# Kernel tuning notes

Measured on AMD Instinct MI355X. Metric: run time of the kernel, lower is better.

The kernel has to match this reference:

```python
import jax, jax.numpy as jnp
import numpy as np

N, E, D, L = 100000, 1600000, 128, 4
NEG_SLOPE = 0.2
LOGSTD_MAX = 10.0


def setup_inputs() -> dict:
    key = jax.random.key(0)
    ks = jax.random.split(key, 20)
    s = 1.0 / np.sqrt(D)
    inp = {
        "x": jax.random.normal(ks[0], (N, D), jnp.float32),
        "edge_index": jax.random.randint(ks[1], (2, E), 0, N, dtype=jnp.int32),
        "eps": jax.random.normal(ks[2], (N, D), jnp.float32),
        # encoder GATv2 stack (4 layers, all inc=D)
        "enc_Wl": jax.random.normal(ks[3], (L, D, D), jnp.float32) * s,
        "enc_Wr": jax.random.normal(ks[4], (L, D, D), jnp.float32) * s,
        "enc_att": jax.random.normal(ks[5], (L, D), jnp.float32) * s,
        "enc_b": jnp.zeros((L, D), jnp.float32),
        # decoder GATv2 stack
        "dec_Wl": jax.random.normal(ks[6], (L, D, D), jnp.float32) * s,
        "dec_Wr": jax.random.normal(ks[7], (L, D, D), jnp.float32) * s,
        "dec_att": jax.random.normal(ks[8], (L, D), jnp.float32) * s,
        "dec_b": jnp.zeros((L, D), jnp.float32),
        # VAE heads
        "W_mu": jax.random.normal(ks[9], (D, D), jnp.float32) * s,
        "b_mu": jnp.zeros((D,), jnp.float32),
        "W_ls": jax.random.normal(ks[10], (D, D), jnp.float32) * s,
        "b_ls": jnp.zeros((D,), jnp.float32),
        # attribute reconstruction head and degree predictor
        "W_out": jax.random.normal(ks[11], (D, D), jnp.float32) * s,
        "b_out": jnp.zeros((D,), jnp.float32),
        "W_deg": jax.random.normal(ks[12], (D, 1), jnp.float32) * s,
        "b_deg": jnp.zeros((1,), jnp.float32),
    }
    return inp


def _gatv2_stack(h, src, dst, Wl, Wr, att, b):
    """Stack of GATv2Conv (heads=1) + gelu, PyG semantics (softmax over incoming edges of dst)."""
    for l in range(Wl.shape[0]):
        xl = h @ Wl[l]  # [N, D] source-side transform
        xr = h @ Wr[l]  # [N, D] target-side transform
        # per-edge GATv2 score: a^T LeakyReLU(xl_j + xr_i)
        e = jax.nn.leaky_relu(xl[src] + xr[dst], NEG_SLOPE) @ att[l]  # [E+N]
        m = jax.ops.segment_max(e, dst, num_segments=N)
        w = jnp.exp(e - m[dst])
        denom = jax.ops.segment_sum(w, dst, num_segments=N)
        alpha = w / denom[dst]
        h = jax.ops.segment_sum(alpha[:, None] * xl[src], dst, num_segments=N) + b[l]
        h = jax.nn.gelu(h, approximate=False)  # torch F.gelu default = exact erf
    return h


def reference(x, edge_index, eps, enc_Wl, enc_Wr, enc_att, enc_b,
              dec_Wl, dec_Wr, dec_att, dec_b,
              W_mu, b_mu, W_ls, b_ls, W_out, b_out, W_deg, b_deg):
    loops = jnp.arange(N, dtype=edge_index.dtype)
    src = jnp.concatenate([edge_index[0], loops])  # add self loops (GATv2Conv default)
    dst = jnp.concatenate([edge_index[1], loops])

    h = _gatv2_stack(x, src, dst, enc_Wl, enc_Wr, enc_att, enc_b)
    mu = h @ W_mu + b_mu
    logstd = jnp.minimum(h @ W_ls + b_ls, LOGSTD_MAX)
    z = mu + eps * jnp.exp(logstd)

    h_dec = _gatv2_stack(z, src, dst, dec_Wl, dec_Wr, dec_att, dec_b)
    x_rec = h_dec @ W_out + b_out
    degree_pred = (z @ W_deg + b_deg)[:, 0]
    return x_rec, z, mu, logstd, degree_pred
```

## Files before the change

kernel.cpp:

```cpp
#include <hip/hip_runtime.h>
#include <math.h>

#define NN 100000
#define MPAD 100096
#define DD 128
#define EE 1600000
#define ET (EE + NN)
#define ND (NN * DD)

#define NBKT 782
#define IPB 16384
#define GSC 104
#define BCAP 6144

typedef short bf16x8 __attribute__((ext_vector_type(8)));
typedef float f32x4 __attribute__((ext_vector_type(4)));

static __device__ __forceinline__ unsigned short f2bf(float f) {
  unsigned int u = __float_as_uint(f);
  u += 0x7FFFu + ((u >> 16) & 1u);
  return (unsigned short)(u >> 16);
}
static __device__ __forceinline__ float bf2f(unsigned short h) {
  return __uint_as_float(((unsigned int)h) << 16);
}
static __device__ __forceinline__ float gelu_exact(float v) {
  return 0.5f * v * (1.f + erff(v * 0.7071067811865476f));
}


__global__ void k_zero_int(int* __restrict__ p, int n) {
  int i = blockIdx.x * blockDim.x + threadIdx.x;
  if (i < n) p[i] = 0;
}

__global__ __launch_bounds__(256) void kb_hist(const int* __restrict__ ei,
                                               int* __restrict__ cnt) {
  __shared__ int lc[NBKT];
  int t = threadIdx.x;
  for (int b = t; b < NBKT; b += 256) lc[b] = 0;
  __syncthreads();
  int i0 = blockIdx.x * IPB;
  int i1 = min(i0 + IPB, ET);
  for (int i = i0 + t; i < i1; i += 256) {
    int dst = (i < EE) ? ei[EE + i] : (i - EE);
    atomicAdd(&lc[dst >> 7], 1);
  }
  __syncthreads();
  for (int b = t; b < NBKT; b += 256) {
    int c = lc[b];
    if (c) atomicAdd(&cnt[b], c);
  }
}

__global__ __launch_bounds__(256) void kb_scan(const int* __restrict__ cnt,
                                               int* __restrict__ off,
                                               int* __restrict__ cur) {
  __shared__ int sh[256];
  int t = threadIdx.x;
  int c[4]; int s = 0;
#pragma unroll
  for (int j = 0; j < 4; ++j) {
    int b = t * 4 + j;
    c[j] = s;
    int v = (b < NBKT) ? cnt[b] : 0;
    s += v;
  }
  sh[t] = s; __syncthreads();
  for (int o = 1; o < 256; o <<= 1) {
    int v = (t >= o) ? sh[t - o] : 0;
    __syncthreads();
    sh[t] += v;
    __syncthreads();
  }
  int excl = sh[t] - s;
#pragma unroll
  for (int j = 0; j < 4; ++j) {
    int b = t * 4 + j;
    if (b < NBKT) { off[b] = excl + c[j]; cur[b] = excl + c[j]; }
  }
  if (t == 255) off[NBKT] = excl + s;
}

__global__ __launch_bounds__(256) void kb_scatter(const int* __restrict__ ei,
                                                  int* __restrict__ cur,
                                                  int* __restrict__ buf) {
  __shared__ int lc[NBKT];
  __shared__ int lb[NBKT];
  int t = threadIdx.x;
  for (int b = t; b < NBKT; b += 256) lc[b] = 0;
  __syncthreads();
  int i0 = blockIdx.x * IPB;
  int i1 = min(i0 + IPB, ET);
  for (int i = i0 + t; i < i1; i += 256) {
    int dst = (i < EE) ? ei[EE + i] : (i - EE);
    atomicAdd(&lc[dst >> 7], 1);
  }
  __syncthreads();
  for (int b = t; b < NBKT; b += 256) {
    int c = lc[b];
    lb[b] = c ? atomicAdd(&cur[b], c) : 0;
    lc[b] = 0;
  }
  __syncthreads();
  for (int i = i0 + t; i < i1; i += 256) {
    int src, dst;
    if (i < EE) { src = ei[i]; dst = ei[EE + i]; } else { src = i - EE; dst = src; }
    int b = dst >> 7;
    int l = atomicAdd(&lc[b], 1);
    buf[lb[b] + l] = src | ((dst & 127) << 17);
  }
}

__global__ __launch_bounds__(256) void kb_fin(const int* __restrict__ buf,
                                              const int* __restrict__ off,
                                              int* __restrict__ csr_src,
                                              int* __restrict__ row_ptr) {
  __shared__ int ebuf[BCAP];
  __shared__ int osrc[BCAP];
  __shared__ int cnt[128], scn[128], lcur[128];
  int b = blockIdx.x;
  int base = off[b];
  int count = min(off[b + 1] - base, BCAP);
  int t = threadIdx.x;
  if (t < 128) { cnt[t] = 0; lcur[t] = 0; }
  __syncthreads();
  for (int i = t; i < count; i += 256) {
    int w = buf[base + i];
    ebuf[i] = w;
    atomicAdd(&cnt[(w >> 17) & 127], 1);
  }
  __syncthreads();
  if (t < 128) scn[t] = cnt[t];
  __syncthreads();
  for (int o = 1; o < 128; o <<= 1) {
    int v = 0;
    if (t < 128 && t >= o) v = scn[t - o];
    __syncthreads();
    if (t < 128) scn[t] += v;
    __syncthreads();
  }
  for (int i = t; i < count; i += 256) {
    int w = ebuf[i];
    int d = (w >> 17) & 127;
    int l = atomicAdd(&lcur[d], 1);
    osrc[(scn[d] - cnt[d]) + l] = w & 0x1FFFF;
  }
  __syncthreads();
  for (int i = t; i < count; i += 256) csr_src[base + i] = osrc[i];
  if (t < 128) {
    int gd = b * 128 + t;
    if (gd <= NN) row_ptr[gd] = base + scn[t] - cnt[t];
  }
}


__global__ __launch_bounds__(256) void k_wconv(const float* __restrict__ encWl,
                                               const float* __restrict__ encWr,
                                               const float* __restrict__ decWl,
                                               const float* __restrict__ decWr,
                                               const float* __restrict__ Wmu,
                                               const float* __restrict__ Wls,
                                               const float* __restrict__ Wout,
                                               unsigned short* __restrict__ wfh,
                                               unsigned short* __restrict__ wfl) {
  int wid = (blockIdx.x * 256 + threadIdx.x) >> 6;
  int lane = threadIdx.x & 63;
  if (wid >= 19 * 32) return;
  int mat = wid >> 5;
  int sub = wid & 31;
  const float* W;
  if (mat < 4) W = encWl + (size_t)mat * 16384;
  else if (mat < 8) W = encWr + (size_t)(mat - 4) * 16384;
  else if (mat < 12) W = decWl + (size_t)(mat - 8) * 16384;
  else if (mat < 16) W = decWr + (size_t)(mat - 12) * 16384;
  else if (mat == 16) W = Wmu;
  else if (mat == 17) W = Wls;
  else W = Wout;
  int t = sub >> 3, c = sub & 7;
  int col = c * 16 + (lane & 15);
  int k0 = t * 32 + (lane >> 4) * 8;
  bf16x8 vh, vl;
#pragma unroll
  for (int j = 0; j < 8; ++j) {
    float w = W[(size_t)(k0 + j) * 128 + col];
    unsigned short h = f2bf(w);
    vh[j] = (short)h;
    vl[j] = (short)f2bf(w - bf2f(h));
  }
  size_t base = ((size_t)wid * 64 + lane) * 8;
  *(bf16x8*)(wfh + base) = vh;
  *(bf16x8*)(wfl + base) = vl;
}


__global__ void k_xconv(const float* __restrict__ x, unsigned short* __restrict__ sh) {
  int i = blockIdx.x * blockDim.x + threadIdx.x;
  if (i >= MPAD * 128 / 8) return;
  size_t base = (size_t)i * 8;
  float v[8];
  if (base < (size_t)ND) {
    float4 f0 = *(const float4*)(x + base);
    float4 f1 = *(const float4*)(x + base + 4);
    v[0] = f0.x; v[1] = f0.y; v[2] = f0.z; v[3] = f0.w;
    v[4] = f1.x; v[5] = f1.y; v[6] = f1.z; v[7] = f1.w;
  } else {
#pragma unroll
    for (int j = 0; j < 8; ++j) v[j] = 0.f;
  }
  bf16x8 vh;
#pragma unroll
  for (int j = 0; j < 8; ++j) vh[j] = (short)f2bf(v[j]);
  *(bf16x8*)(sh + base) = vh;
}


__global__ __launch_bounds__(512, 4) void k_mmL(const unsigned short* __restrict__ Ah,
                                                const unsigned short* __restrict__ w1,
                                                const unsigned short* __restrict__ w2,
                                                unsigned short* __restrict__ o1,
                                                unsigned short* __restrict__ o2) {
  __shared__ float lds[128 * 132];
  unsigned short* lw = (unsigned short*)lds;
  int tid = threadIdx.x;
  {
    int4* d = (int4*)lw;
    const int4* s1 = (const int4*)w1;
    const int4* s2 = (const int4*)w2;
#pragma unroll
    for (int i = 0; i < 4; ++i) {
      d[tid + i * 512] = s1[tid + i * 512];
      d[2048 + tid + i * 512] = s2[tid + i * 512];
    }
  }
  int wv = tid >> 6, lane = tid & 63;
  int lrow = lane & 15, lk = lane >> 4;
  int rbase = blockIdx.x * 128 + wv * 16;

  bf16x8 a_h[4];
  const unsigned short* ap = Ah + (size_t)(rbase + lrow) * 128 + lk * 8;
#pragma unroll
  for (int t = 0; t < 4; ++t) a_h[t] = *(const bf16x8*)(ap + t * 32);
  __syncthreads();

  f32x4 acc1[8], acc2[8];
#pragma unroll
  for (int c = 0; c < 8; ++c) {
    acc1[c] = (f32x4){0.f, 0.f, 0.f, 0.f};
    acc2[c] = (f32x4){0.f, 0.f, 0.f, 0.f};
  }
#pragma unroll
  for (int t = 0; t < 4; ++t) {
#pragma unroll
    for (int c = 0; c < 8; ++c) {
      int fo = ((t * 8 + c) * 64 + lane) * 8;
      bf16x8 wf1 = *(const bf16x8*)(lw + fo);
      bf16x8 wf2 = *(const bf16x8*)(lw + 16384 + fo);
      acc1[c] = __builtin_amdgcn_mfma_f32_16x16x32_bf16(a_h[t], wf1, acc1[c], 0, 0, 0);
      acc2[c] = __builtin_amdgcn_mfma_f32_16x16x32_bf16(a_h[t], wf2, acc2[c], 0, 0, 0);
    }
  }
  __syncthreads();

  int lr = tid >> 2, cb = (tid & 3) << 5;
  size_t o = ((size_t)blockIdx.x * 128 + lr) * 128 + cb;

#pragma unroll
  for (int out = 0; out < 2; ++out) {
#pragma unroll
    for (int c = 0; c < 8; ++c)
#pragma unroll
      for (int r = 0; r < 4; ++r)
        lds[(wv * 16 + lk * 4 + r) * 132 + c * 16 + lrow] = out ? acc2[c][r] : acc1[c][r];
    __syncthreads();
    {
      unsigned short* dst = out ? o2 : o1;
      const float* sp = &lds[lr * 132 + cb];
#pragma unroll
      for (int i = 0; i < 4; ++i) {
        union { unsigned short u[8]; int4 v; } pk;
#pragma unroll
        for (int j = 0; j < 8; ++j) pk.u[j] = f2bf(sp[i * 8 + j]);
        *(int4*)&dst[o + i * 8] = pk.v;
      }
    }
    __syncthreads();
  }
}


__global__ __launch_bounds__(512, 3) void k_mmH(const unsigned short* Ah,
                                                const unsigned short* Al,
                                                const unsigned short* __restrict__ w1h,
                                                const unsigned short* __restrict__ w1l,
                                                const unsigned short* __restrict__ w2h,
                                                const unsigned short* __restrict__ w2l,
                                                const float* __restrict__ b1,
                                                const float* __restrict__ b2,
                                                const float* __restrict__ eps,
                                                const float* __restrict__ Wd,
                                                const float* __restrict__ bd,
                                                float* __restrict__ mu,
                                                float* __restrict__ logstd,
                                                float* __restrict__ Z,
                                                unsigned short* Zh,
                                                float* __restrict__ degp) {
  __shared__ float lds[128 * 132];
  unsigned short* lw = (unsigned short*)lds;
  int tid = threadIdx.x;
  int wv = tid >> 6, lane = tid & 63;
  int lrow = lane & 15, lk = lane >> 4;
  int rbase = blockIdx.x * 128 + wv * 16;

  {
    int4* d = (int4*)lw;
#pragma unroll
    for (int i = 0; i < 4; ++i) {
      d[tid + i * 512] = ((const int4*)w1h)[tid + i * 512];
      d[2048 + tid + i * 512] = ((const int4*)w1l)[tid + i * 512];
    }
  }
  bf16x8 a_h[4], a_l[4];
  const unsigned short* ap = Ah + (size_t)(rbase + lrow) * 128 + lk * 8;
  const unsigned short* alp = Al + (size_t)(rbase + lrow) * 128 + lk * 8;
#pragma unroll
  for (int t = 0; t < 4; ++t) {
    a_h[t] = *(const bf16x8*)(ap + t * 32);
    a_l[t] = *(const bf16x8*)(alp + t * 32);
  }
  __syncthreads();

  f32x4 acc1[8];
#pragma unroll
  for (int c = 0; c < 8; ++c) acc1[c] = (f32x4){0.f, 0.f, 0.f, 0.f};
#pragma unroll
  for (int t = 0; t < 4; ++t) {
#pragma unroll
    for (int c = 0; c < 8; ++c) {
      int fo = ((t * 8 + c) * 64 + lane) * 8;
      bf16x8 wh = *(const bf16x8*)(lw + fo);
      bf16x8 wl = *(const bf16x8*)(lw + 16384 + fo);
      acc1[c] = __builtin_amdgcn_mfma_f32_16x16x32_bf16(a_h[t], wh, acc1[c], 0, 0, 0);
      acc1[c] = __builtin_amdgcn_mfma_f32_16x16x32_bf16(a_l[t], wh, acc1[c], 0, 0, 0);
      acc1[c] = __builtin_amdgcn_mfma_f32_16x16x32_bf16(a_h[t], wl, acc1[c], 0, 0, 0);
    }
  }
  __syncthreads();

  {
    int4* d = (int4*)lw;
#pragma unroll
    for (int i = 0; i < 4; ++i) {
      d[tid + i * 512] = ((const int4*)w2h)[tid + i * 512];
      d[2048 + tid + i * 512] = ((const int4*)w2l)[tid + i * 512];
    }
  }
  __syncthreads();

  f32x4 acc2[8];
#pragma unroll
  for (int c = 0; c < 8; ++c) acc2[c] = (f32x4){0.f, 0.f, 0.f, 0.f};
#pragma unroll
  for (int t = 0; t < 4; ++t) {
#pragma unroll
    for (int c = 0; c < 8; ++c) {
      int fo = ((t * 8 + c) * 64 + lane) * 8;
      bf16x8 wh = *(const bf16x8*)(lw + fo);
      bf16x8 wl = *(const bf16x8*)(lw + 16384 + fo);
      acc2[c] = __builtin_amdgcn_mfma_f32_16x16x32_bf16(a_h[t], wh, acc2[c], 0, 0, 0);
      acc2[c] = __builtin_amdgcn_mfma_f32_16x16x32_bf16(a_l[t], wh, acc2[c], 0, 0, 0);
      acc2[c] = __builtin_amdgcn_mfma_f32_16x16x32_bf16(a_h[t], wl, acc2[c], 0, 0, 0);
    }
  }
  __syncthreads();

  int lr = tid >> 2, cb = (tid & 3) << 5;
  int grow = blockIdx.x * 128 + lr;
  size_t o = (size_t)grow * 128 + cb;

#pragma unroll
  for (int c = 0; c < 8; ++c)
#pragma unroll
    for (int r = 0; r < 4; ++r)
      lds[(wv * 16 + lk * 4 + r) * 132 + c * 16 + lrow] = acc1[c][r];
  __syncthreads();
  float4 mureg[8];
  if (grow < NN) {
    const float* sp = &lds[lr * 132 + cb];
#pragma unroll
    for (int i = 0; i < 8; ++i) {
      float4 v = *(const float4*)(sp + i * 4);
      float4 b4 = *(const float4*)&b1[cb + i * 4];
      v.x += b4.x; v.y += b4.y; v.z += b4.z; v.w += b4.w;
      mureg[i] = v;
      *(float4*)&mu[o + i * 4] = v;
    }
  }
  __syncthreads();
#pragma unroll
  for (int c = 0; c < 8; ++c)
#pragma unroll
    for (int r = 0; r < 4; ++r)
      lds[(wv * 16 + lk * 4 + r) * 132 + c * 16 + lrow] = acc2[c][r];
  __syncthreads();
  float s_deg = 0.f;
  if (grow < NN) {
    const float* sp = &lds[lr * 132 + cb];
#pragma unroll
    for (int i = 0; i < 8; ++i) {
      float4 v = *(const float4*)(sp + i * 4);
      float4 b4 = *(const float4*)&b2[cb + i * 4];
      float4 ls;
      ls.x = fminf(v.x + b4.x, 10.f);
      ls.y = fminf(v.y + b4.y, 10.f);
      ls.z = fminf(v.z + b4.z, 10.f);
      ls.w = fminf(v.w + b4.w, 10.f);
      *(float4*)&logstd[o + i * 4] = ls;
      float4 e4 = *(const float4*)&eps[o + i * 4];
      float4 z4;
      z4.x = fmaf(e4.x, expf(ls.x), mureg[i].x);
      z4.y = fmaf(e4.y, expf(ls.y), mureg[i].y);
      z4.z = fmaf(e4.z, expf(ls.z), mureg[i].z);
      z4.w = fmaf(e4.w, expf(ls.w), mureg[i].w);
      *(float4*)&Z[o + i * 4] = z4;
      ushort4 hh;
      hh.x = f2bf(z4.x); hh.y = f2bf(z4.y); hh.z = f2bf(z4.z); hh.w = f2bf(z4.w);
      *(ushort4*)&Zh[o + i * 4] = hh;
      float4 wd = *(const float4*)&Wd[cb + i * 4];
      s_deg += z4.x * wd.x + z4.y * wd.y + z4.z * wd.z + z4.w * wd.w;
    }
  }
  s_deg += __shfl_xor(s_deg, 1);
  s_deg += __shfl_xor(s_deg, 2);
  if (grow < NN && (tid & 3) == 0) degp[grow] = s_deg + bd[0];
}


__global__ __launch_bounds__(512, 4) void k_mmO(const unsigned short* __restrict__ Ah,
                                                const unsigned short* __restrict__ Al,
                                                const unsigned short* __restrict__ wh,
                                                const unsigned short* __restrict__ wl,
                                                const float* __restrict__ bias,
                                                float* __restrict__ C) {
  __shared__ float lds[128 * 132];
  unsigned short* lw = (unsigned short*)lds;
  int tid = threadIdx.x;
  {
    int4* d = (int4*)lw;
#pragma unroll
    for (int i = 0; i < 4; ++i) {
      d[tid + i * 512] = ((const int4*)wh)[tid + i * 512];
      d[2048 + tid + i * 512] = ((const int4*)wl)[tid + i * 512];
    }
  }
  int wv = tid >> 6, lane = tid & 63;
  int lrow = lane & 15, lk = lane >> 4;
  int rbase = blockIdx.x * 128 + wv * 16;

  bf16x8 a_h[4], a_l[4];
  const unsigned short* ap = Ah + (size_t)(rbase + lrow) * 128 + lk * 8;
  const unsigned short* alp = Al + (size_t)(rbase + lrow) * 128 + lk * 8;
#pragma unroll
  for (int t = 0; t < 4; ++t) {
    a_h[t] = *(const bf16x8*)(ap + t * 32);
    a_l[t] = *(const bf16x8*)(alp + t * 32);
  }
  __syncthreads();

  f32x4 acc[8];
#pragma unroll
  for (int c = 0; c < 8; ++c) acc[c] = (f32x4){0.f, 0.f, 0.f, 0.f};
#pragma unroll
  for (int t = 0; t < 4; ++t) {
#pragma unroll
    for (int c = 0; c < 8; ++c) {
      int fo = ((t * 8 + c) * 64 + lane) * 8;
      bf16x8 whf = *(const bf16x8*)(lw + fo);
      bf16x8 wlf = *(const bf16x8*)(lw + 16384 + fo);
      acc[c] = __builtin_amdgcn_mfma_f32_16x16x32_bf16(a_h[t], whf, acc[c], 0, 0, 0);
      acc[c] = __builtin_amdgcn_mfma_f32_16x16x32_bf16(a_l[t], whf, acc[c], 0, 0, 0);
      acc[c] = __builtin_amdgcn_mfma_f32_16x16x32_bf16(a_h[t], wlf, acc[c], 0, 0, 0);
    }
  }
  __syncthreads();

#pragma unroll
  for (int c = 0; c < 8; ++c)
#pragma unroll
    for (int r = 0; r < 4; ++r)
      lds[(wv * 16 + lk * 4 + r) * 132 + c * 16 + lrow] = acc[c][r];
  __syncthreads();
  int lr = tid >> 2, cb = (tid & 3) << 5;
  int grow = blockIdx.x * 128 + lr;
  if (grow < NN) {
    size_t o = (size_t)grow * 128 + cb;
    const float* sp = &lds[lr * 132 + cb];
#pragma unroll
    for (int i = 0; i < 8; ++i) {
      float4 v = *(const float4*)(sp + i * 4);
      float4 b4 = *(const float4*)&bias[cb + i * 4];
      v.x += b4.x; v.y += b4.y; v.z += b4.z; v.w += b4.w;
      *(float4*)&C[o + i * 4] = v;
    }
  }
}


template <int WLO>
__global__ __launch_bounds__(256) void k_gat_agg(const unsigned short* __restrict__ gxl,
                                                 const unsigned short* __restrict__ gxr,
                                                 const float* __restrict__ att,
                                                 const float* __restrict__ bias,
                                                 const int* __restrict__ row_ptr,
                                                 const int* __restrict__ csr_src,
                                                 unsigned short* __restrict__ sh,
                                                 unsigned short* __restrict__ sl) {
  int gid = blockIdx.x * blockDim.x + threadIdx.x;
  int row = gid >> 6;
  int lane = gid & 63;
  if (row >= NN) return;
  int g = lane >> 4, j = lane & 15;
  int dbase = j * 8;

  float a[8], r[8];
  {
    float4 a0 = *(const float4*)&att[dbase];
    float4 a1 = *(const float4*)&att[dbase + 4];
    a[0] = a0.x; a[1] = a0.y; a[2] = a0.z; a[3] = a0.w;
    a[4] = a1.x; a[5] = a1.y; a[6] = a1.z; a[7] = a1.w;
    bf16x8 rv = *(const bf16x8*)&gxr[(size_t)row * 128 + dbase];
#pragma unroll
    for (int k = 0; k < 8; ++k) r[k] = bf2f((unsigned short)rv[k]);
  }

  float m = -INFINITY, d = 0.f;
  float acc[8] = {0.f, 0.f, 0.f, 0.f, 0.f, 0.f, 0.f, 0.f};
  int p0 = row_ptr[row], p1 = row_ptr[row + 1];

  for (int p = p0 + g; p < p1; p += 4) {
    int s = csr_src[p];
    bf16x8 xv = *(const bf16x8*)&gxl[(size_t)s * 128 + dbase];
    float v[8];
#pragma unroll
    for (int k = 0; k < 8; ++k) v[k] = bf2f((unsigned short)xv[k]);

    float e = 0.f;
#pragma unroll
    for (int k = 0; k < 8; ++k) {
      float t0 = v[k] + r[k];
      t0 = fmaxf(t0, 0.2f * t0);
      e = fmaf(t0, a[k], e);
    }
    e += __shfl_xor(e, 1);
    e += __shfl_xor(e, 2);
    e += __shfl_xor(e, 4);
    e += __shfl_xor(e, 8);

    float mn = fmaxf(m, e);
    float scl = __expf(m - mn);
    float w = __expf(e - mn);
    d = d * scl + w;
#pragma unroll
    for (int k = 0; k < 8; ++k) acc[k] = acc[k] * scl + w * v[k];
    m = mn;
  }

  float mo = fmaxf(m, __shfl_xor(m, 16));
  mo = fmaxf(mo, __shfl_xor(mo, 32));
  float scl = __expf(m - mo);
  d *= scl;
  d += __shfl_xor(d, 16);
  d += __shfl_xor(d, 32);
#pragma unroll
  for (int k = 0; k < 8; ++k) {
    acc[k] *= scl;
    acc[k] += __shfl_xor(acc[k], 16);
    acc[k] += __shfl_xor(acc[k], 32);
  }

  if (g == 0) {
    float inv = 1.f / d;
    float4 b0 = *(const float4*)&bias[dbase];
    float4 b1v = *(const float4*)&bias[dbase + 4];
    float bb[8] = {b0.x, b0.y, b0.z, b0.w, b1v.x, b1v.y, b1v.z, b1v.w};
    bf16x8 vh, vl;
#pragma unroll
    for (int k = 0; k < 8; ++k) {
      float h = gelu_exact(acc[k] * inv + bb[k]);
      unsigned short hi = f2bf(h);
      vh[k] = (short)hi;
      if (WLO) vl[k] = (short)f2bf(h - bf2f(hi));
    }
    *(bf16x8*)(sh + (size_t)row * 128 + dbase) = vh;
    if (WLO) *(bf16x8*)(sl + (size_t)row * 128 + dbase) = vl;
  }
}


static inline char* take(char*& p, size_t bytes) {
  char* r = p;
  p += (bytes + 255) & ~(size_t)255;
  return r;
}

extern "C" void kernel_launch(void* const* d_in, const int* in_sizes, int n_in,
                              void* d_out, int out_size, void* d_ws, size_t ws_size,
                              hipStream_t stream) {
  const float* x      = (const float*)d_in[0];
  const int*   ei     = (const int*)d_in[1];
  const float* eps    = (const float*)d_in[2];
  const float* encWl  = (const float*)d_in[3];
  const float* encWr  = (const float*)d_in[4];
  const float* encAtt = (const float*)d_in[5];
  const float* encB   = (const float*)d_in[6];
  const float* decWl  = (const float*)d_in[7];
  const float* decWr  = (const float*)d_in[8];
  const float* decAtt = (const float*)d_in[9];
  const float* decB   = (const float*)d_in[10];
  const float* W_mu   = (const float*)d_in[11];
  const float* b_mu   = (const float*)d_in[12];
  const float* W_ls   = (const float*)d_in[13];
  const float* b_ls   = (const float*)d_in[14];
  const float* W_out  = (const float*)d_in[15];
  const float* b_out  = (const float*)d_in[16];
  const float* W_deg  = (const float*)d_in[17];
  const float* b_deg  = (const float*)d_in[18];

  float* out    = (float*)d_out;
  float* x_rec  = out;
  float* z      = out + (size_t)ND;
  float* mu     = out + (size_t)2 * ND;
  float* logstd = out + (size_t)3 * ND;
  float* degp   = out + (size_t)4 * ND;

  char* p = (char*)d_ws;
  int* bktcnt  = (int*)take(p, 1024 * 4);
  int* bktoff  = (int*)take(p, 1024 * 4);
  int* bktcur  = (int*)take(p, 1024 * 4);
  int* ebuf_g  = (int*)take(p, (size_t)ET * 4);
  int* row_ptr = (int*)take(p, (size_t)(NN + 1) * 4);
  int* csr_src = (int*)take(p, (size_t)ET * 4);
  unsigned short* gxl  = (unsigned short*)take(p, (size_t)MPAD * 128 * 2);
  unsigned short* gxr  = (unsigned short*)take(p, (size_t)MPAD * 128 * 2);
  unsigned short* stgh = (unsigned short*)take(p, (size_t)MPAD * 128 * 2);
  unsigned short* stgl = (unsigned short*)take(p, (size_t)MPAD * 128 * 2);
  unsigned short* wfh  = (unsigned short*)take(p, (size_t)19 * 16384 * 2);
  unsigned short* wfl  = (unsigned short*)take(p, (size_t)19 * 16384 * 2);

  const int gMM   = MPAD / 128;
  const int gWave = (NN * 64 + 255) / 256;
  const int gXC   = (MPAD * 128 / 8 + 255) / 256;

  k_zero_int<<<4, 256, 0, stream>>>(bktcnt, 1024);
  kb_hist<<<GSC, 256, 0, stream>>>(ei, bktcnt);
  kb_scan<<<1, 256, 0, stream>>>(bktcnt, bktoff, bktcur);
  kb_scatter<<<GSC, 256, 0, stream>>>(ei, bktcur, ebuf_g);
  kb_fin<<<NBKT, 256, 0, stream>>>(ebuf_g, bktoff, csr_src, row_ptr);

  k_wconv<<<152, 256, 0, stream>>>(encWl, encWr, decWl, decWr, W_mu, W_ls, W_out, wfh, wfl);
  k_xconv<<<gXC, 256, 0, stream>>>(x, stgh);

  const size_t WM = 16384;
  for (int l = 0; l < 4; ++l) {
    k_mmL<<<gMM, 512, 0, stream>>>(stgh,
                                   wfh + (size_t)l * WM, wfh + (size_t)(4 + l) * WM,
                                   gxl, gxr);
    if (l < 3)
      k_gat_agg<0><<<gWave, 256, 0, stream>>>(gxl, gxr, encAtt + (size_t)l * DD,
                                              encB + (size_t)l * DD, row_ptr, csr_src,
                                              stgh, stgl);
    else
      k_gat_agg<1><<<gWave, 256, 0, stream>>>(gxl, gxr, encAtt + (size_t)l * DD,
                                              encB + (size_t)l * DD, row_ptr, csr_src,
                                              stgh, stgl);
  }

  k_mmH<<<gMM, 512, 0, stream>>>(stgh, stgl,
                                 wfh + (size_t)16 * WM, wfl + (size_t)16 * WM,
                                 wfh + (size_t)17 * WM, wfl + (size_t)17 * WM,
                                 b_mu, b_ls, eps, W_deg, b_deg,
                                 mu, logstd, z, stgh, degp);

  for (int l = 0; l < 4; ++l) {
    k_mmL<<<gMM, 512, 0, stream>>>(stgh,
                                   wfh + (size_t)(8 + l) * WM, wfh + (size_t)(12 + l) * WM,
                                   gxl, gxr);
    if (l < 3)
      k_gat_agg<0><<<gWave, 256, 0, stream>>>(gxl, gxr, decAtt + (size_t)l * DD,
                                              decB + (size_t)l * DD, row_ptr, csr_src,
                                              stgh, stgl);
    else
      k_gat_agg<1><<<gWave, 256, 0, stream>>>(gxl, gxr, decAtt + (size_t)l * DD,
                                              decB + (size_t)l * DD, row_ptr, csr_src,
                                              stgh, stgl);
  }

  k_mmO<<<gMM, 512, 0, stream>>>(stgh, stgl,
                                 wfh + (size_t)18 * WM, wfl + (size_t)18 * WM,
                                 b_out, x_rec);
}
```

Baseline: 1.372 ms.

## Fuse x conversion into first GEMM, double GEMM rows, unroll GAT edge loop, drop low split

Removes the standalone fp32-to-bf16 conversion kernel by converting x inside the first layer's GEMM. The layer GEMM now does 256 rows per block, each wave handling two 16-row tiles so weight fragments from LDS are reused, with launch bounds lowered to 2. The GAT aggregation loop handles two edges per iteration to expose more memory-level parallelism. The final output GEMM drops the low-part activation term, and the last decoder layer now uses the bf16-only aggregation variant, which lowers output precision.

Measured after the change: 1.438 ms. 1.05x slower.

```diff
diff --git a/kernel.cpp b/kernel.cpp
--- a/kernel.cpp
+++ b/kernel.cpp
@@ -194,28 +194,9 @@
 }
 
 
-__global__ void k_xconv(const float* __restrict__ x, unsigned short* __restrict__ sh) {
-  int i = blockIdx.x * blockDim.x + threadIdx.x;
-  if (i >= MPAD * 128 / 8) return;
-  size_t base = (size_t)i * 8;
-  float v[8];
-  if (base < (size_t)ND) {
-    float4 f0 = *(const float4*)(x + base);
-    float4 f1 = *(const float4*)(x + base + 4);
-    v[0] = f0.x; v[1] = f0.y; v[2] = f0.z; v[3] = f0.w;
-    v[4] = f1.x; v[5] = f1.y; v[6] = f1.z; v[7] = f1.w;
-  } else {
-#pragma unroll
-    for (int j = 0; j < 8; ++j) v[j] = 0.f;
-  }
-  bf16x8 vh;
-#pragma unroll
-  for (int j = 0; j < 8; ++j) vh[j] = (short)f2bf(v[j]);
-  *(bf16x8*)(sh + base) = vh;
-}
-
-
-__global__ __launch_bounds__(512, 4) void k_mmL(const unsigned short* __restrict__ Ah,
+template <int RF32>
+__global__ __launch_bounds__(512, 2) void k_mmL(const unsigned short* __restrict__ Ah,
+                                                const float* __restrict__ Xf,
                                                 const unsigned short* __restrict__ w1,
                                                 const unsigned short* __restrict__ w2,
                                                 unsigned short* __restrict__ o1,
@@ -235,20 +216,44 @@
   }
   int wv = tid >> 6, lane = tid & 63;
   int lrow = lane & 15, lk = lane >> 4;
-  int rbase = blockIdx.x * 128 + wv * 16;
-
-  bf16x8 a_h[4];
-  const unsigned short* ap = Ah + (size_t)(rbase + lrow) * 128 + lk * 8;
-#pragma unroll
-  for (int t = 0; t < 4; ++t) a_h[t] = *(const bf16x8*)(ap + t * 32);
-  __syncthreads();
-
-  f32x4 acc1[8], acc2[8];
-#pragma unroll
-  for (int c = 0; c < 8; ++c) {
-    acc1[c] = (f32x4){0.f, 0.f, 0.f, 0.f};
-    acc2[c] = (f32x4){0.f, 0.f, 0.f, 0.f};
-  }
+  int rbase = blockIdx.x * 256 + wv * 32;
+
+  bf16x8 a_h[2][4];
+#pragma unroll
+  for (int n = 0; n < 2; ++n) {
+    int row = rbase + n * 16 + lrow;
+    if (RF32) {
+#pragma unroll
+      for (int t = 0; t < 4; ++t) {
+        float4 f0 = {0.f, 0.f, 0.f, 0.f}, f1 = {0.f, 0.f, 0.f, 0.f};
+        if (row < NN) {
+          const float* xp = Xf + (size_t)row * 128 + t * 32 + lk * 8;
+          f0 = *(const float4*)xp;
+          f1 = *(const float4*)(xp + 4);
+        }
+        bf16x8 v;
+        v[0] = (short)f2bf(f0.x); v[1] = (short)f2bf(f0.y);
+        v[2] = (short)f2bf(f0.z); v[3] = (short)f2bf(f0.w);
+        v[4] = (short)f2bf(f1.x); v[5] = (short)f2bf(f1.y);
+        v[6] = (short)f2bf(f1.z); v[7] = (short)f2bf(f1.w);
+        a_h[n][t] = v;
+      }
+    } else {
+      const unsigned short* ap = Ah + (size_t)row * 128 + lk * 8;
+#pragma unroll
+      for (int t = 0; t < 4; ++t) a_h[n][t] = *(const bf16x8*)(ap + t * 32);
+    }
+  }
+  __syncthreads();
+
+  f32x4 acc1[2][8], acc2[2][8];
+#pragma unroll
+  for (int n = 0; n < 2; ++n)
+#pragma unroll
+    for (int c = 0; c < 8; ++c) {
+      acc1[n][c] = (f32x4){0.f, 0.f, 0.f, 0.f};
+      acc2[n][c] = (f32x4){0.f, 0.f, 0.f, 0.f};
+    }
 #pragma unroll
   for (int t = 0; t < 4; ++t) {
 #pragma unroll
@@ -256,35 +261,46 @@
       int fo = ((t * 8 + c) * 64 + lane) * 8;
       bf16x8 wf1 = *(const bf16x8*)(lw + fo);
       bf16x8 wf2 = *(const bf16x8*)(lw + 16384 + fo);
-      acc1[c] = __builtin_amdgcn_mfma_f32_16x16x32_bf16(a_h[t], wf1, acc1[c], 0, 0, 0);
-      acc2[c] = __builtin_amdgcn_mfma_f32_16x16x32_bf16(a_h[t], wf2, acc2[c], 0, 0, 0);
+#pragma unroll
+      for (int n = 0; n < 2; ++n) {
+        acc1[n][c] = __builtin_amdgcn_mfma_f32_16x16x32_bf16(a_h[n][t], wf1, acc1[n][c], 0, 0, 0);
+        acc2[n][c] = __builtin_amdgcn_mfma_f32_16x16x32_bf16(a_h[n][t], wf2, acc2[n][c], 0, 0, 0);
+      }
     }
   }
   __syncthreads();
 
   int lr = tid >> 2, cb = (tid & 3) << 5;
-  size_t o = ((size_t)blockIdx.x * 128 + lr) * 128 + cb;
-
-#pragma unroll
-  for (int out = 0; out < 2; ++out) {
-#pragma unroll
-    for (int c = 0; c < 8; ++c)
-#pragma unroll
-      for (int r = 0; r < 4; ++r)
-        lds[(wv * 16 + lk * 4 + r) * 132 + c * 16 + lrow] = out ? acc2[c][r] : acc1[c][r];
-    __syncthreads();
-    {
-      unsigned short* dst = out ? o2 : o1;
-      const float* sp = &lds[lr * 132 + cb];
-#pragma unroll
-      for (int i = 0; i < 4; ++i) {
-        union { unsigned short u[8]; int4 v; } pk;
-#pragma unroll
-        for (int j = 0; j < 8; ++j) pk.u[j] = f2bf(sp[i * 8 + j]);
-        *(int4*)&dst[o + i * 8] = pk.v;
+#pragma unroll
+  for (int h = 0; h < 2; ++h) {
+#pragma unroll
+    for (int out = 0; out < 2; ++out) {
+      if ((wv >> 2) == h) {
+        int lrb = (wv & 3) * 32;
+#pragma unroll
+        for (int n = 0; n < 2; ++n)
+#pragma unroll
+          for (int c = 0; c < 8; ++c)
+#pragma unroll
+            for (int r = 0; r < 4; ++r)
+              lds[(lrb + n * 16 + lk * 4 + r) * 132 + c * 16 + lrow] =
+                  out ? acc2[n][c][r] : acc1[n][c][r];
       }
-    }
-    __syncthreads();
+      __syncthreads();
+      {
+        unsigned short* dst = out ? o2 : o1;
+        size_t o = ((size_t)blockIdx.x * 256 + h * 128 + lr) * 128 + cb;
+        const float* sp = &lds[lr * 132 + cb];
+#pragma unroll
+        for (int i = 0; i < 4; ++i) {
+          union { unsigned short u[8]; int4 v; } pk;
+#pragma unroll
+          for (int j = 0; j < 8; ++j) pk.u[j] = f2bf(sp[i * 8 + j]);
+          *(int4*)&dst[o + i * 8] = pk.v;
+        }
+      }
+      __syncthreads();
+    }
   }
 }
 
@@ -437,7 +453,6 @@
 
 
 __global__ __launch_bounds__(512, 4) void k_mmO(const unsigned short* __restrict__ Ah,
-                                                const unsigned short* __restrict__ Al,
                                                 const unsigned short* __restrict__ wh,
                                                 const unsigned short* __restrict__ wl,
                                                 const float* __restrict__ bias,
@@ -457,14 +472,10 @@
   int lrow = lane & 15, lk = lane >> 4;
   int rbase = blockIdx.x * 128 + wv * 16;
 
-  bf16x8 a_h[4], a_l[4];
+  bf16x8 a_h[4];
   const unsigned short* ap = Ah + (size_t)(rbase + lrow) * 128 + lk * 8;
-  const unsigned short* alp = Al + (size_t)(rbase + lrow) * 128 + lk * 8;
-#pragma unroll
-  for (int t = 0; t < 4; ++t) {
-    a_h[t] = *(const bf16x8*)(ap + t * 32);
-    a_l[t] = *(const bf16x8*)(alp + t * 32);
-  }
+#pragma unroll
+  for (int t = 0; t < 4; ++t) a_h[t] = *(const bf16x8*)(ap + t * 32);
   __syncthreads();
 
   f32x4 acc[8];
@@ -478,7 +489,6 @@
       bf16x8 whf = *(const bf16x8*)(lw + fo);
       bf16x8 wlf = *(const bf16x8*)(lw + 16384 + fo);
       acc[c] = __builtin_amdgcn_mfma_f32_16x16x32_bf16(a_h[t], whf, acc[c], 0, 0, 0);
-      acc[c] = __builtin_amdgcn_mfma_f32_16x16x32_bf16(a_l[t], whf, acc[c], 0, 0, 0);
       acc[c] = __builtin_amdgcn_mfma_f32_16x16x32_bf16(a_h[t], wlf, acc[c], 0, 0, 0);
     }
   }
@@ -537,31 +547,47 @@
   float acc[8] = {0.f, 0.f, 0.f, 0.f, 0.f, 0.f, 0.f, 0.f};
   int p0 = row_ptr[row], p1 = row_ptr[row + 1];
 
-  for (int p = p0 + g; p < p1; p += 4) {
-    int s = csr_src[p];
-    bf16x8 xv = *(const bf16x8*)&gxl[(size_t)s * 128 + dbase];
-    float v[8];
-#pragma unroll
-    for (int k = 0; k < 8; ++k) v[k] = bf2f((unsigned short)xv[k]);
-
-    float e = 0.f;
+  for (int p = p0 + g; p < p1; p += 8) {
+    int pb = p + 4;
+    bool hb = pb < p1;
+    int sa = csr_src[p];
+    int sb = csr_src[hb ? pb : p];
+    bf16x8 xa = *(const bf16x8*)&gxl[(size_t)sa * 128 + dbase];
+    bf16x8 xb = *(const bf16x8*)&gxl[(size_t)sb * 128 + dbase];
+    float va[8], vb[8];
 #pragma unroll
     for (int k = 0; k < 8; ++k) {
-      float t0 = v[k] + r[k];
-      t0 = fmaxf(t0, 0.2f * t0);
-      e = fmaf(t0, a[k], e);
-    }
-    e += __shfl_xor(e, 1);
-    e += __shfl_xor(e, 2);
-    e += __shfl_xor(e, 4);
-    e += __shfl_xor(e, 8);
-
-    float mn = fmaxf(m, e);
+      va[k] = bf2f((unsigned short)xa[k]);
+      vb[k] = bf2f((unsigned short)xb[k]);
+    }
+    float ea = 0.f, eb = 0.f;
+#pragma unroll
+    for (int k = 0; k < 8; ++k) {
+      float ta = va[k] + r[k];
+      ta = fmaxf(ta, 0.2f * ta);
+      ea = fmaf(ta, a[k], ea);
+      float tb = vb[k] + r[k];
+      tb = fmaxf(tb, 0.2f * tb);
+      eb = fmaf(tb, a[k], eb);
+    }
+    ea += __shfl_xor(ea, 1);
+    eb += __shfl_xor(eb, 1);
+    ea += __shfl_xor(ea, 2);
+    eb += __shfl_xor(eb, 2);
+    ea += __shfl_xor(ea, 4);
+    eb += __shfl_xor(eb, 4);
+    ea += __shfl_xor(ea, 8);
+    eb += __shfl_xor(eb, 8);
+    if (!hb) eb = -INFINITY;
+
+    float mn = fmaxf(m, fmaxf(ea, eb));
     float scl = __expf(m - mn);
-    float w = __expf(e - mn);
-    d = d * scl + w;
-#pragma unroll
-    for (int k = 0; k < 8; ++k) acc[k] = acc[k] * scl + w * v[k];
+    float wa = __expf(ea - mn);
+    float wb = __expf(eb - mn);
+    d = d * scl + wa + wb;
+#pragma unroll
+    for (int k = 0; k < 8; ++k)
+      acc[k] = fmaf(acc[k], scl, fmaf(wa, va[k], wb * vb[k]));
     m = mn;
   }
 
@@ -647,9 +673,9 @@
   unsigned short* wfh  = (unsigned short*)take(p, (size_t)19 * 16384 * 2);
   unsigned short* wfl  = (unsigned short*)take(p, (size_t)19 * 16384 * 2);
 
+  const int gMML  = MPAD / 256;
   const int gMM   = MPAD / 128;
   const int gWave = (NN * 64 + 255) / 256;
-  const int gXC   = (MPAD * 128 / 8 + 255) / 256;
 
   k_zero_int<<<4, 256, 0, stream>>>(bktcnt, 1024);
   kb_hist<<<GSC, 256, 0, stream>>>(ei, bktcnt);
@@ -658,13 +684,17 @@
   kb_fin<<<NBKT, 256, 0, stream>>>(ebuf_g, bktoff, csr_src, row_ptr);
 
   k_wconv<<<152, 256, 0, stream>>>(encWl, encWr, decWl, decWr, W_mu, W_ls, W_out, wfh, wfl);
-  k_xconv<<<gXC, 256, 0, stream>>>(x, stgh);
 
   const size_t WM = 16384;
   for (int l = 0; l < 4; ++l) {
-    k_mmL<<<gMM, 512, 0, stream>>>(stgh,
-                                   wfh + (size_t)l * WM, wfh + (size_t)(4 + l) * WM,
-                                   gxl, gxr);
+    if (l == 0)
+      k_mmL<1><<<gMML, 512, 0, stream>>>(nullptr, x,
+                                         wfh + (size_t)l * WM, wfh + (size_t)(4 + l) * WM,
+                                         gxl, gxr);
+    else
+      k_mmL<0><<<gMML, 512, 0, stream>>>(stgh, nullptr,
+                                         wfh + (size_t)l * WM, wfh + (size_t)(4 + l) * WM,
+                                         gxl, gxr);
     if (l < 3)
       k_gat_agg<0><<<gWave, 256, 0, stream>>>(gxl, gxr, encAtt + (size_t)l * DD,
                                               encB + (size_t)l * DD, row_ptr, csr_src,
@@ -682,20 +712,15 @@
                                  mu, logstd, z, stgh, degp);
 
   for (int l = 0; l < 4; ++l) {
-    k_mmL<<<gMM, 512, 0, stream>>>(stgh,
-                                   wfh + (size_t)(8 + l) * WM, wfh + (size_t)(12 + l) * WM,
-                                   gxl, gxr);
-    if (l < 3)
-      k_gat_agg<0><<<gWave, 256, 0, stream>>>(gxl, gxr, decAtt + (size_t)l * DD,
-                                              decB + (size_t)l * DD, row_ptr, csr_src,
-                                              stgh, stgl);
-    else
-      k_gat_agg<1><<<gWave, 256, 0, stream>>>(gxl, gxr, decAtt + (size_t)l * DD,
-                                              decB + (size_t)l * DD, row_ptr, csr_src,
-                                              stgh, stgl);
-  }
-
-  k_mmO<<<gMM, 512, 0, stream>>>(stgh, stgl,
+    k_mmL<0><<<gMML, 512, 0, stream>>>(stgh, nullptr,
+                                       wfh + (size_t)(8 + l) * WM, wfh + (size_t)(12 + l) * WM,
+                                       gxl, gxr);
+    k_gat_agg<0><<<gWave, 256, 0, stream>>>(gxl, gxr, decAtt + (size_t)l * DD,
+                                            decB + (size_t)l * DD, row_ptr, csr_src,
+                                            stgh, stgl);
+  }
+
+  k_mmO<<<gMM, 512, 0, stream>>>(stgh,
                                  wfh + (size_t)18 * WM, wfl + (size_t)18 * WM,
                                  b_out, x_rec);
 }
```

## Merge CSR histogram into scatter, fuse x conversion, drop low-part output GEMM

Applied to the files above, without the earlier changes.

The CSR build drops the separate histogram pass and scatters edges straight into fixed-capacity per-bucket slack slots (SCAP entries each), with the scan moved after the scatter. The fp32 to bf16 conversion of x is fused into the first matmul's operand load, removing a separate kernel. The last decoder layer now uses the bf16-only aggregation variant, and the output GEMM drops the low-part activation MFMA, which reduces precision. Buckets holding more than SCAP edges would silently drop edges.

New measurement: 1.335 ms. -2.7%, faster.

```diff
diff --git a/kernel.cpp b/kernel.cpp
--- a/kernel.cpp
+++ b/kernel.cpp
@@ -11,7 +11,7 @@
 #define NBKT 782
 #define IPB 16384
 #define GSC 104
-#define BCAP 6144
+#define SCAP 4096
 
 typedef short bf16x8 __attribute__((ext_vector_type(8)));
 typedef float f32x4 __attribute__((ext_vector_type(4)));
@@ -34,9 +34,11 @@
   if (i < n) p[i] = 0;
 }
 
-__global__ __launch_bounds__(256) void kb_hist(const int* __restrict__ ei,
-                                               int* __restrict__ cnt) {
+__global__ __launch_bounds__(256) void kb_scatter(const int* __restrict__ ei,
+                                                  int* __restrict__ cnt,
+                                                  int* __restrict__ slack) {
   __shared__ int lc[NBKT];
+  __shared__ int lb[NBKT];
   int t = threadIdx.x;
   for (int b = t; b < NBKT; b += 256) lc[b] = 0;
   __syncthreads();
@@ -49,13 +51,22 @@
   __syncthreads();
   for (int b = t; b < NBKT; b += 256) {
     int c = lc[b];
-    if (c) atomicAdd(&cnt[b], c);
+    lb[b] = c ? atomicAdd(&cnt[b], c) : 0;
+    lc[b] = 0;
+  }
+  __syncthreads();
+  for (int i = i0 + t; i < i1; i += 256) {
+    int src, dst;
+    if (i < EE) { src = ei[i]; dst = ei[EE + i]; } else { src = i - EE; dst = src; }
+    int b = dst >> 7;
+    int l = atomicAdd(&lc[b], 1);
+    int pos = lb[b] + l;
+    if (pos < SCAP) slack[(size_t)b * SCAP + pos] = src | ((dst & 127) << 17);
   }
 }
 
 __global__ __launch_bounds__(256) void kb_scan(const int* __restrict__ cnt,
-                                               int* __restrict__ off,
-                                               int* __restrict__ cur) {
+                                               int* __restrict__ off) {
   __shared__ int sh[256];
   int t = threadIdx.x;
   int c[4]; int s = 0;
@@ -77,56 +88,27 @@
 #pragma unroll
   for (int j = 0; j < 4; ++j) {
     int b = t * 4 + j;
-    if (b < NBKT) { off[b] = excl + c[j]; cur[b] = excl + c[j]; }
+    if (b < NBKT) off[b] = excl + c[j];
   }
   if (t == 255) off[NBKT] = excl + s;
 }
 
-__global__ __launch_bounds__(256) void kb_scatter(const int* __restrict__ ei,
-                                                  int* __restrict__ cur,
-                                                  int* __restrict__ buf) {
-  __shared__ int lc[NBKT];
-  __shared__ int lb[NBKT];
-  int t = threadIdx.x;
-  for (int b = t; b < NBKT; b += 256) lc[b] = 0;
-  __syncthreads();
-  int i0 = blockIdx.x * IPB;
-  int i1 = min(i0 + IPB, ET);
-  for (int i = i0 + t; i < i1; i += 256) {
-    int dst = (i < EE) ? ei[EE + i] : (i - EE);
-    atomicAdd(&lc[dst >> 7], 1);
-  }
-  __syncthreads();
-  for (int b = t; b < NBKT; b += 256) {
-    int c = lc[b];
-    lb[b] = c ? atomicAdd(&cur[b], c) : 0;
-    lc[b] = 0;
-  }
-  __syncthreads();
-  for (int i = i0 + t; i < i1; i += 256) {
-    int src, dst;
-    if (i < EE) { src = ei[i]; dst = ei[EE + i]; } else { src = i - EE; dst = src; }
-    int b = dst >> 7;
-    int l = atomicAdd(&lc[b], 1);
-    buf[lb[b] + l] = src | ((dst & 127) << 17);
-  }
-}
-
-__global__ __launch_bounds__(256) void kb_fin(const int* __restrict__ buf,
+__global__ __launch_bounds__(256) void kb_fin(const int* __restrict__ slack,
                                               const int* __restrict__ off,
                                               int* __restrict__ csr_src,
                                               int* __restrict__ row_ptr) {
-  __shared__ int ebuf[BCAP];
-  __shared__ int osrc[BCAP];
+  __shared__ int ebuf[SCAP];
+  __shared__ int osrc[SCAP];
   __shared__ int cnt[128], scn[128], lcur[128];
   int b = blockIdx.x;
   int base = off[b];
-  int count = min(off[b + 1] - base, BCAP);
+  int count = min(off[b + 1] - base, SCAP);
   int t = threadIdx.x;
+  const int* in = slack + (size_t)b * SCAP;
   if (t < 128) { cnt[t] = 0; lcur[t] = 0; }
   __syncthreads();
   for (int i = t; i < count; i += 256) {
-    int w = buf[base + i];
+    int w = in[i];
     ebuf[i] = w;
     atomicAdd(&cnt[(w >> 17) & 127], 1);
   }
@@ -194,28 +176,9 @@
 }
 
 
-__global__ void k_xconv(const float* __restrict__ x, unsigned short* __restrict__ sh) {
-  int i = blockIdx.x * blockDim.x + threadIdx.x;
-  if (i >= MPAD * 128 / 8) return;
-  size_t base = (size_t)i * 8;
-  float v[8];
-  if (base < (size_t)ND) {
-    float4 f0 = *(const float4*)(x + base);
-    float4 f1 = *(const float4*)(x + base + 4);
-    v[0] = f0.x; v[1] = f0.y; v[2] = f0.z; v[3] = f0.w;
-    v[4] = f1.x; v[5] = f1.y; v[6] = f1.z; v[7] = f1.w;
-  } else {
-#pragma unroll
-    for (int j = 0; j < 8; ++j) v[j] = 0.f;
-  }
-  bf16x8 vh;
-#pragma unroll
-  for (int j = 0; j < 8; ++j) vh[j] = (short)f2bf(v[j]);
-  *(bf16x8*)(sh + base) = vh;
-}
-
-
+template <int RF32>
 __global__ __launch_bounds__(512, 4) void k_mmL(const unsigned short* __restrict__ Ah,
+                                                const float* __restrict__ Xf,
                                                 const unsigned short* __restrict__ w1,
                                                 const unsigned short* __restrict__ w2,
                                                 unsigned short* __restrict__ o1,
@@ -236,11 +199,30 @@
   int wv = tid >> 6, lane = tid & 63;
   int lrow = lane & 15, lk = lane >> 4;
   int rbase = blockIdx.x * 128 + wv * 16;
+  int row = rbase + lrow;
 
   bf16x8 a_h[4];
-  const unsigned short* ap = Ah + (size_t)(rbase + lrow) * 128 + lk * 8;
-#pragma unroll
-  for (int t = 0; t < 4; ++t) a_h[t] = *(const bf16x8*)(ap + t * 32);
+  if (RF32) {
+#pragma unroll
+    for (int t = 0; t < 4; ++t) {
+      float4 f0 = {0.f, 0.f, 0.f, 0.f}, f1 = {0.f, 0.f, 0.f, 0.f};
+      if (row < NN) {
+        const float* xp = Xf + (size_t)row * 128 + t * 32 + lk * 8;
+        f0 = *(const float4*)xp;
+        f1 = *(const float4*)(xp + 4);
+      }
+      bf16x8 v;
+      v[0] = (short)f2bf(f0.x); v[1] = (short)f2bf(f0.y);
+      v[2] = (short)f2bf(f0.z); v[3] = (short)f2bf(f0.w);
+      v[4] = (short)f2bf(f1.x); v[5] = (short)f2bf(f1.y);
+      v[6] = (short)f2bf(f1.z); v[7] = (short)f2bf(f1.w);
+      a_h[t] = v;
+    }
+  } else {
+    const unsigned short* ap = Ah + (size_t)row * 128 + lk * 8;
+#pragma unroll
+    for (int t = 0; t < 4; ++t) a_h[t] = *(const bf16x8*)(ap + t * 32);
+  }
   __syncthreads();
 
   f32x4 acc1[8], acc2[8];
@@ -437,7 +419,6 @@
 
 
 __global__ __launch_bounds__(512, 4) void k_mmO(const unsigned short* __restrict__ Ah,
-                                                const unsigned short* __restrict__ Al,
                                                 const unsigned short* __restrict__ wh,
                                                 const unsigned short* __restrict__ wl,
                                                 const float* __restrict__ bias,
@@ -457,14 +438,10 @@
   int lrow = lane & 15, lk = lane >> 4;
   int rbase = blockIdx.x * 128 + wv * 16;
 
-  bf16x8 a_h[4], a_l[4];
+  bf16x8 a_h[4];
   const unsigned short* ap = Ah + (size_t)(rbase + lrow) * 128 + lk * 8;
-  const unsigned short* alp = Al + (size_t)(rbase + lrow) * 128 + lk * 8;
-#pragma unroll
-  for (int t = 0; t < 4; ++t) {
-    a_h[t] = *(const bf16x8*)(ap + t * 32);
-    a_l[t] = *(const bf16x8*)(alp + t * 32);
-  }
+#pragma unroll
+  for (int t = 0; t < 4; ++t) a_h[t] = *(const bf16x8*)(ap + t * 32);
   __syncthreads();
 
   f32x4 acc[8];
@@ -478,7 +455,6 @@
       bf16x8 whf = *(const bf16x8*)(lw + fo);
       bf16x8 wlf = *(const bf16x8*)(lw + 16384 + fo);
       acc[c] = __builtin_amdgcn_mfma_f32_16x16x32_bf16(a_h[t], whf, acc[c], 0, 0, 0);
-      acc[c] = __builtin_amdgcn_mfma_f32_16x16x32_bf16(a_l[t], whf, acc[c], 0, 0, 0);
       acc[c] = __builtin_amdgcn_mfma_f32_16x16x32_bf16(a_h[t], wlf, acc[c], 0, 0, 0);
     }
   }
@@ -636,8 +612,7 @@
   char* p = (char*)d_ws;
   int* bktcnt  = (int*)take(p, 1024 * 4);
   int* bktoff  = (int*)take(p, 1024 * 4);
-  int* bktcur  = (int*)take(p, 1024 * 4);
-  int* ebuf_g  = (int*)take(p, (size_t)ET * 4);
+  int* slack   = (int*)take(p, (size_t)NBKT * SCAP * 4);
   int* row_ptr = (int*)take(p, (size_t)(NN + 1) * 4);
   int* csr_src = (int*)take(p, (size_t)ET * 4);
   unsigned short* gxl  = (unsigned short*)take(p, (size_t)MPAD * 128 * 2);
@@ -649,22 +624,24 @@
 
   const int gMM   = MPAD / 128;
   const int gWave = (NN * 64 + 255) / 256;
-  const int gXC   = (MPAD * 128 / 8 + 255) / 256;
 
   k_zero_int<<<4, 256, 0, stream>>>(bktcnt, 1024);
-  kb_hist<<<GSC, 256, 0, stream>>>(ei, bktcnt);
-  kb_scan<<<1, 256, 0, stream>>>(bktcnt, bktoff, bktcur);
-  kb_scatter<<<GSC, 256, 0, stream>>>(ei, bktcur, ebuf_g);
-  kb_fin<<<NBKT, 256, 0, stream>>>(ebuf_g, bktoff, csr_src, row_ptr);
+  kb_scatter<<<GSC, 256, 0, stream>>>(ei, bktcnt, slack);
+  kb_scan<<<1, 256, 0, stream>>>(bktcnt, bktoff);
+  kb_fin<<<NBKT, 256, 0, stream>>>(slack, bktoff, csr_src, row_ptr);
 
   k_wconv<<<152, 256, 0, stream>>>(encWl, encWr, decWl, decWr, W_mu, W_ls, W_out, wfh, wfl);
-  k_xconv<<<gXC, 256, 0, stream>>>(x, stgh);
 
   const size_t WM = 16384;
   for (int l = 0; l < 4; ++l) {
-    k_mmL<<<gMM, 512, 0, stream>>>(stgh,
-                                   wfh + (size_t)l * WM, wfh + (size_t)(4 + l) * WM,
-                                   gxl, gxr);
+    if (l == 0)
+      k_mmL<1><<<gMM, 512, 0, stream>>>(nullptr, x,
+                                        wfh + (size_t)l * WM, wfh + (size_t)(4 + l) * WM,
+                                        gxl, gxr);
+    else
+      k_mmL<0><<<gMM, 512, 0, stream>>>(stgh, nullptr,
+                                        wfh + (size_t)l * WM, wfh + (size_t)(4 + l) * WM,
+                                        gxl, gxr);
     if (l < 3)
       k_gat_agg<0><<<gWave, 256, 0, stream>>>(gxl, gxr, encAtt + (size_t)l * DD,
                                               encB + (size_t)l * DD, row_ptr, csr_src,
@@ -682,20 +659,15 @@
                                  mu, logstd, z, stgh, degp);
 
   for (int l = 0; l < 4; ++l) {
-    k_mmL<<<gMM, 512, 0, stream>>>(stgh,
-                                   wfh + (size_t)(8 + l) * WM, wfh + (size_t)(12 + l) * WM,
-                                   gxl, gxr);
-    if (l < 3)
-      k_gat_agg<0><<<gWave, 256, 0, stream>>>(gxl, gxr, decAtt + (size_t)l * DD,
-                                              decB + (size_t)l * DD, row_ptr, csr_src,
-                                              stgh, stgl);
-    else
-      k_gat_agg<1><<<gWave, 256, 0, stream>>>(gxl, gxr, decAtt + (size_t)l * DD,
-                                              decB + (size_t)l * DD, row_ptr, csr_src,
-                                              stgh, stgl);
-  }
-
-  k_mmO<<<gMM, 512, 0, stream>>>(stgh, stgl,
+    k_mmL<0><<<gMM, 512, 0, stream>>>(stgh, nullptr,
+                                      wfh + (size_t)(8 + l) * WM, wfh + (size_t)(12 + l) * WM,
+                                      gxl, gxr);
+    k_gat_agg<0><<<gWave, 256, 0, stream>>>(gxl, gxr, decAtt + (size_t)l * DD,
+                                            decB + (size_t)l * DD, row_ptr, csr_src,
+                                            stgh, stgl);
+  }
+
+  k_mmO<<<gMM, 512, 0, stream>>>(stgh,
                                  wfh + (size_t)18 * WM, wfl + (size_t)18 * WM,
                                  b_out, x_rec);
 }
```
